# Performance work log

Measured on AMD Instinct MI355X. Metric: run time of the kernel, lower is better.

## Reference

```python
import jax, jax.numpy as jnp
import numpy as np

B, M, H = 8, 1024, 1024
NH, HD = 16, 64  # num_heads, head_dim


def setup_inputs() -> dict:
    key = jax.random.key(0)
    ks = jax.random.split(key, 16)
    s = 0.02
    def lin(k, din, dout):
        k1, k2 = jax.random.split(k)
        return (jax.random.normal(k1, (din, dout), jnp.float32) * s,
                jax.random.normal(k2, (dout,), jnp.float32) * s)
    x = jax.random.normal(ks[0], (B, M, H), jnp.float32)
    Wq, bq = lin(ks[1], H, H)
    Wk, bk = lin(ks[2], H, H)
    Wv, bv = lin(ks[3], H, H)
    Wg, bg = lin(ks[4], H, H)
    Wo, bo = lin(ks[5], H, H)
    Wu1, bu1 = lin(ks[6], H, H // 4)
    Wu2, bu2 = lin(ks[7], H // 4, 1)
    return dict(x=x, Wq=Wq, bq=bq, Wk=Wk, bk=bk, Wv=Wv, bv=bv, Wg=Wg, bg=bg,
                Wo=Wo, bo=bo, Wu1=Wu1, bu1=bu1, Wu2=Wu2, bu2=bu2)


def reference(x, Wq, bq, Wk, bk, Wv, bv, Wg, bg, Wo, bo, Wu1, bu1, Wu2, bu2):
    b, m, _ = x.shape
    shp = lambda t: t.reshape(b, m, NH, HD)
    q = shp(x @ Wq + bq)
    k = shp(x @ Wk + bk)
    v = shp(x @ Wv + bv)
    g = jax.nn.sigmoid(shp(x @ Wg + bg))
    scores = jnp.einsum('bmhd,bnhd->bhmn', q, k) / (HD ** 0.5)
    # modality uncertainty: Linear -> ReLU -> Linear -> Softplus, squeeze(-1)
    sigma = jax.nn.softplus(jax.nn.relu(x @ Wu1 + bu1) @ Wu2 + bu2)[..., 0] + 1e-6
    # sigma_pair: [b, 1, m, 1] * [b, 1, 1, m] -> broadcast over heads
    scores = scores / (sigma[:, None, :, None] * sigma[:, None, None, :])
    attn = jax.nn.softmax(scores, axis=-1)
    ctx = jnp.einsum('bhmn,bnhd->bmhd', attn, v) * g
    fused = ctx.reshape(b, m, H)
    z = fused.mean(axis=1) @ Wo + bo
    return (z, attn, sigma)
```

## Files before the change

### kernel.cpp

```cpp
#include <hip/hip_runtime.h>
#include <math.h>

#define BB 8
#define MM 1024
#define HH 1024
#define NH 16
#define HD 64
#define NCAT 4352
#define ROWS (BB*MM)

typedef unsigned short ushortT;
typedef __attribute__((ext_vector_type(8))) short bf16x8;
typedef __attribute__((ext_vector_type(4))) float f32x4;

__device__ __forceinline__ unsigned short f2bf(float f) {
    union { float f; unsigned int u; } v; v.f = f;
    unsigned int u = v.u;
    unsigned int r = (u + 0x7fffu + ((u >> 16) & 1u)) >> 16;
    return (unsigned short)r;
}
__device__ __forceinline__ float bf2f(unsigned short s) {
    union { unsigned int u; float f; } v; v.u = ((unsigned int)s) << 16;
    return v.f;
}

__device__ __forceinline__ void async_copy16(const void* g, void* l) {
    __builtin_amdgcn_global_load_lds(
        (const __attribute__((address_space(1))) unsigned int*)g,
        (__attribute__((address_space(3))) unsigned int*)l, 16, 0, 0);
}

__global__ void cast_x_k(const float* __restrict__ x, ushortT* __restrict__ Xb) {
    size_t i = ((size_t)blockIdx.x * 256 + threadIdx.x) * 4;
    float4 v = *(const float4*)&x[i];
    ushort4 o;
    o.x = f2bf(v.x); o.y = f2bf(v.y); o.z = f2bf(v.z); o.w = f2bf(v.w);
    *(ushort4*)&Xb[i] = o;
}

__global__ void wtrans_k(const float* __restrict__ Wq, const float* __restrict__ Wk,
                         const float* __restrict__ Wv, const float* __restrict__ Wg,
                         const float* __restrict__ Wu1, ushortT* __restrict__ Wt) {
    __shared__ float t[64][65];
    int n0 = blockIdx.x * 64, k0 = blockIdx.y * 64;
    const float* src; int ncols; int nloc0;
    if (n0 < 1024)      { src = Wq;  nloc0 = n0;        ncols = 1024; }
    else if (n0 < 2048) { src = Wk;  nloc0 = n0 - 1024; ncols = 1024; }
    else if (n0 < 3072) { src = Wv;  nloc0 = n0 - 2048; ncols = 1024; }
    else if (n0 < 4096) { src = Wg;  nloc0 = n0 - 3072; ncols = 1024; }
    else                { src = Wu1; nloc0 = n0 - 4096; ncols = 256;  }
    int tid = threadIdx.x, c = tid & 63, rq = tid >> 6;
#pragma unroll
    for (int i = 0; i < 16; i++) {
        int k = i * 4 + rq;
        t[k][c] = src[(size_t)(k0 + k) * ncols + nloc0 + c];
    }
    __syncthreads();
#pragma unroll
    for (int i = 0; i < 16; i++) {
        int nn = i * 4 + rq;
        Wt[(size_t)(n0 + nn) * 1024 + k0 + c] = f2bf(t[c][nn]);
    }
}

__global__ void biascat_k(const float* __restrict__ bq, const float* __restrict__ bk,
                          const float* __restrict__ bv, const float* __restrict__ bg,
                          const float* __restrict__ bu1, float* __restrict__ bc) {
    int i = blockIdx.x * 256 + threadIdx.x;
    if (i >= NCAT) return;
    float v;
    if (i < 1024) v = bq[i];
    else if (i < 2048) v = bk[i - 1024];
    else if (i < 3072) v = bv[i - 2048];
    else if (i < 4096) v = bg[i - 3072];
    else v = bu1[i - 4096];
    bc[i] = v;
}

__global__ __launch_bounds__(256, 2) void gemm_proj_k(
    const ushortT* __restrict__ Xb, const ushortT* __restrict__ Wt,
    const float* __restrict__ biascat, ushortT* __restrict__ Ycat) {
    __shared__ ushortT lA[128 * 64];
    __shared__ ushortT lB[128 * 64];
    const int tid = threadIdx.x;
    const int wave = tid >> 6;
    const int lane = tid & 63;
    const int quad = lane >> 4;
    const int l16 = lane & 15;
    const int m0 = blockIdx.y * 128;
    const int n0 = blockIdx.x * 128;
    const int wr = (wave >> 1) * 64;
    const int wc = (wave & 1) * 64;

    f32x4 acc[16];
#pragma unroll
    for (int i = 0; i < 16; i++) acc[i] = (f32x4){0.f, 0.f, 0.f, 0.f};

    for (int k0 = 0; k0 < 1024; k0 += 64) {
#pragma unroll
        for (int i = 0; i < 4; i++) {
            int c = wave * 256 + i * 64 + lane;
            int row = c >> 3, kc = c & 7;
            async_copy16(&Xb[(size_t)(m0 + row) * 1024 + k0 + kc * 8], &lA[c * 8]);
            async_copy16(&Wt[(size_t)(n0 + row) * 1024 + k0 + kc * 8], &lB[c * 8]);
        }
        __syncthreads();
#pragma unroll
        for (int kk = 0; kk < 64; kk += 32) {
            bf16x8 a[4], b[4];
#pragma unroll
            for (int i = 0; i < 4; i++)
                a[i] = *(const bf16x8*)&lA[(wr + i * 16 + l16) * 64 + kk + quad * 8];
#pragma unroll
            for (int j = 0; j < 4; j++)
                b[j] = *(const bf16x8*)&lB[(wc + j * 16 + l16) * 64 + kk + quad * 8];
#pragma unroll
            for (int i = 0; i < 4; i++)
#pragma unroll
                for (int j = 0; j < 4; j++)
                    acc[i * 4 + j] = __builtin_amdgcn_mfma_f32_16x16x32_bf16(
                        a[i], b[j], acc[i * 4 + j], 0, 0, 0);
        }
        __syncthreads();
    }

#pragma unroll
    for (int i = 0; i < 4; i++) {
#pragma unroll
        for (int j = 0; j < 4; j++) {
            int col = n0 + wc + j * 16 + l16;
            float bias = biascat[col];
#pragma unroll
            for (int r = 0; r < 4; r++) {
                int row = m0 + wr + i * 16 + quad * 4 + r;
                float y = acc[i * 4 + j][r] + bias;
                if (n0 < 1024) y *= 0.125f;
                else if (n0 < 3072) {  }
                else if (n0 < 4096) y = 1.f / (1.f + __expf(-y));
                else y = fmaxf(y, 0.f);
                Ycat[(size_t)row * NCAT + col] = f2bf(y);
            }
        }
    }
}

__global__ void vtrans_k(const ushortT* __restrict__ Ycat, ushortT* __restrict__ Vt) {
    __shared__ ushortT t[64][72];
    int n0 = blockIdx.x * 64, h = blockIdx.y, b = blockIdx.z;
    const ushortT* Vbase = Ycat + (size_t)(b * MM) * NCAT + 2048 + h * HD;
    int tid = threadIdx.x, c = tid & 63, rq = tid >> 6;
#pragma unroll
    for (int i = 0; i < 16; i++) {
        int n = i * 4 + rq;
        t[n][c] = Vbase[(size_t)(n0 + n) * NCAT + c];
    }
    __syncthreads();
    ushortT* out = Vt + (size_t)((b * NH + h) * HD) * MM;
#pragma unroll
    for (int i = 0; i < 16; i++) {
        int d = i * 4 + rq;
        out[(size_t)d * MM + n0 + c] = t[c][d];
    }
}

__global__ void sigma_k(const ushortT* __restrict__ Ycat, const float* __restrict__ Wu2,
                        const float* __restrict__ bu2, float* __restrict__ out_sigma,
                        float* __restrict__ rsig) {
    int row = blockIdx.x * 4 + (threadIdx.x >> 6);
    int lane = threadIdx.x & 63;
    const ushortT* u = Ycat + (size_t)row * NCAT + 4096;
    ushort4 uv = *(const ushort4*)(u + lane * 4);
    float4 wv = *(const float4*)(Wu2 + lane * 4);
    float acc = bf2f(uv.x) * wv.x + bf2f(uv.y) * wv.y + bf2f(uv.z) * wv.z + bf2f(uv.w) * wv.w;
#pragma unroll
    for (int d = 1; d < 64; d <<= 1) acc += __shfl_xor(acc, d, 64);
    if (lane == 0) {
        float y = acc + bu2[0];
        float sp = (y > 20.f) ? y : log1pf(__expf(y));
        float s = sp + 1e-6f;
        out_sigma[row] = s;
        rsig[row] = 1.f / s;
    }
}

__global__ __launch_bounds__(256, 2) void attn_k(
    const ushortT* __restrict__ Ycat, const ushortT* __restrict__ Vt,
    const float* __restrict__ rsig, float* __restrict__ attn_out,
    float* __restrict__ meanacc) {
    __shared__ ushortT lQ[64 * 64];
    __shared__ ushortT lK[64 * 64];
    __shared__ ushortT lV[64 * 64];
    __shared__ ushortT lP[4][16 * 64];
    __shared__ float lrs[1024];

    const int tid = threadIdx.x, wave = tid >> 6, lane = tid & 63;
    const int quad = lane >> 4, l16 = lane & 15;
    const int m0 = blockIdx.x * 64, h = blockIdx.y, b = blockIdx.z;

    const ushortT* Qbase = Ycat + (size_t)(b * MM) * NCAT + h * HD;
    const ushortT* Kbase = Ycat + (size_t)(b * MM) * NCAT + 1024 + h * HD;
    const ushortT* Gbase = Ycat + (size_t)(b * MM) * NCAT + 3072 + h * HD;
    const ushortT* Vbase = Vt + (size_t)((b * NH + h) * HD) * MM;

    for (int i = tid; i < 1024; i += 256) lrs[i] = rsig[b * MM + i];
#pragma unroll
    for (int i = 0; i < 2; i++) {
        int c = wave * 128 + i * 64 + lane;
        int row = c >> 3, kc = c & 7;
        async_copy16(&Qbase[(size_t)(m0 + row) * NCAT + kc * 8], &lQ[c * 8]);
    }
    __syncthreads();

    bf16x8 qa[2];
#pragma unroll
    for (int kk = 0; kk < 2; kk++)
        qa[kk] = *(const bf16x8*)&lQ[(wave * 16 + l16) * 64 + kk * 32 + quad * 8];
    float rm[4];
#pragma unroll
    for (int r = 0; r < 4; r++) rm[r] = lrs[m0 + wave * 16 + quad * 4 + r];

    float Mx[4], L[4];
#pragma unroll
    for (int r = 0; r < 4; r++) { Mx[r] = -1e30f; L[r] = 0.f; }

    for (int n0 = 0; n0 < MM; n0 += 64) {
#pragma unroll
        for (int i = 0; i < 2; i++) {
            int c = wave * 128 + i * 64 + lane;
            int row = c >> 3, kc = c & 7;
            async_copy16(&Kbase[(size_t)(n0 + row) * NCAT + kc * 8], &lK[c * 8]);
        }
        __syncthreads();
        f32x4 s[4];
#pragma unroll
        for (int j = 0; j < 4; j++) {
            bf16x8 b0 = *(const bf16x8*)&lK[(j * 16 + l16) * 64 + quad * 8];
            bf16x8 b1 = *(const bf16x8*)&lK[(j * 16 + l16) * 64 + 32 + quad * 8];
            f32x4 t = (f32x4){0.f, 0.f, 0.f, 0.f};
            t = __builtin_amdgcn_mfma_f32_16x16x32_bf16(qa[0], b0, t, 0, 0, 0);
            t = __builtin_amdgcn_mfma_f32_16x16x32_bf16(qa[1], b1, t, 0, 0, 0);
            float rn = lrs[n0 + j * 16 + l16];
#pragma unroll
            for (int r = 0; r < 4; r++) t[r] *= rm[r] * rn;
            s[j] = t;
        }
        __syncthreads();
#pragma unroll
        for (int r = 0; r < 4; r++) {
            float mx = fmaxf(fmaxf(s[0][r], s[1][r]), fmaxf(s[2][r], s[3][r]));
#pragma unroll
            for (int d = 1; d < 16; d <<= 1) mx = fmaxf(mx, __shfl_xor(mx, d, 16));
            float nm = fmaxf(Mx[r], mx);
            float sum = __expf(s[0][r] - nm) + __expf(s[1][r] - nm) +
                        __expf(s[2][r] - nm) + __expf(s[3][r] - nm);
#pragma unroll
            for (int d = 1; d < 16; d <<= 1) sum += __shfl_xor(sum, d, 16);
            L[r] = L[r] * __expf(Mx[r] - nm) + sum;
            Mx[r] = nm;
        }
    }

    float Li[4];
#pragma unroll
    for (int r = 0; r < 4; r++) Li[r] = 1.f / L[r];
    f32x4 ctx[4];
#pragma unroll
    for (int j = 0; j < 4; j++) ctx[j] = (f32x4){0.f, 0.f, 0.f, 0.f};
    float* attn_base = attn_out + ((size_t)((b * NH + h) * MM + m0)) * MM;
    ushortT* Pw = lP[wave];

    for (int n0 = 0; n0 < MM; n0 += 64) {
#pragma unroll
        for (int i = 0; i < 2; i++) {
            int c = wave * 128 + i * 64 + lane;
            int row = c >> 3, kc = c & 7;
            async_copy16(&Kbase[(size_t)(n0 + row) * NCAT + kc * 8], &lK[c * 8]);
            async_copy16(&Vbase[(size_t)row * MM + n0 + kc * 8], &lV[c * 8]);
        }
        __syncthreads();
#pragma unroll
        for (int j = 0; j < 4; j++) {
            bf16x8 b0 = *(const bf16x8*)&lK[(j * 16 + l16) * 64 + quad * 8];
            bf16x8 b1 = *(const bf16x8*)&lK[(j * 16 + l16) * 64 + 32 + quad * 8];
            f32x4 t = (f32x4){0.f, 0.f, 0.f, 0.f};
            t = __builtin_amdgcn_mfma_f32_16x16x32_bf16(qa[0], b0, t, 0, 0, 0);
            t = __builtin_amdgcn_mfma_f32_16x16x32_bf16(qa[1], b1, t, 0, 0, 0);
            float rn = lrs[n0 + j * 16 + l16];
#pragma unroll
            for (int r = 0; r < 4; r++) {
                float p = __expf(t[r] * rm[r] * rn - Mx[r]) * Li[r];
                int mloc = wave * 16 + quad * 4 + r;
                attn_base[(size_t)mloc * MM + n0 + j * 16 + l16] = p;
                Pw[(quad * 4 + r) * 64 + j * 16 + l16] = f2bf(p);
            }
        }
        __syncthreads();
#pragma unroll
        for (int kk = 0; kk < 2; kk++) {
            bf16x8 pa = *(const bf16x8*)&Pw[l16 * 64 + kk * 32 + quad * 8];
#pragma unroll
            for (int j = 0; j < 4; j++) {
                bf16x8 vb = *(const bf16x8*)&lV[(j * 16 + l16) * 64 + kk * 32 + quad * 8];
                ctx[j] = __builtin_amdgcn_mfma_f32_16x16x32_bf16(pa, vb, ctx[j], 0, 0, 0);
            }
        }
        __syncthreads();
    }

#pragma unroll
    for (int j = 0; j < 4; j++) {
        int d = j * 16 + l16;
        float sum = 0.f;
#pragma unroll
        for (int r = 0; r < 4; r++) {
            int mrow = m0 + wave * 16 + quad * 4 + r;
            float gv = bf2f(Gbase[(size_t)mrow * NCAT + d]);
            sum += ctx[j][r] * gv;
        }
        sum += __shfl_xor(sum, 16, 64);
        sum += __shfl_xor(sum, 32, 64);
        if (quad == 0)
            atomicAdd(&meanacc[b * HH + h * HD + d], sum);
    }
}

__global__ void z_k(const float* __restrict__ meanacc, const float* __restrict__ Wo,
                    const float* __restrict__ bo, float* __restrict__ z) {
    int n = blockIdx.x * 256 + threadIdx.x;
    int b = blockIdx.y;
    int k0 = blockIdx.z * 64;
    float acc = 0.f;
#pragma unroll 4
    for (int k = k0; k < k0 + 64; k++)
        acc = fmaf(meanacc[b * HH + k], Wo[(size_t)k * HH + n], acc);
    float v = acc * (1.f / 1024.f);
    if (blockIdx.z == 0) v += bo[n];
    atomicAdd(&z[b * HH + n], v);
}

extern "C" void kernel_launch(void* const* d_in, const int* in_sizes, int n_in,
                              void* d_out, int out_size, void* d_ws, size_t ws_size,
                              hipStream_t stream) {
    const float* x   = (const float*)d_in[0];
    const float* Wq  = (const float*)d_in[1];
    const float* bq  = (const float*)d_in[2];
    const float* Wk  = (const float*)d_in[3];
    const float* bk  = (const float*)d_in[4];
    const float* Wv  = (const float*)d_in[5];
    const float* bv  = (const float*)d_in[6];
    const float* Wg  = (const float*)d_in[7];
    const float* bg  = (const float*)d_in[8];
    const float* Wo  = (const float*)d_in[9];
    const float* bo  = (const float*)d_in[10];
    const float* Wu1 = (const float*)d_in[11];
    const float* bu1 = (const float*)d_in[12];
    const float* Wu2 = (const float*)d_in[13];
    const float* bu2 = (const float*)d_in[14];

    char* ws = (char*)d_ws;
    ushortT* Xb      = (ushortT*)(ws + 0);
    ushortT* Wt      = (ushortT*)(ws + 16777216);
    float*   biascat = (float*)  (ws + 25690112);
    ushortT* Ycat    = (ushortT*)(ws + 25707520);
    ushortT* Vt      = (ushortT*)(ws + 97010688);
    float*   rsig    = (float*)  (ws + 113787904);
    float*   meanacc = (float*)  (ws + 113820672);

    float* z_out     = (float*)d_out;
    float* attn_out  = (float*)d_out + 8192;
    float* sigma_out = (float*)d_out + 8192 + 134217728;

    hipMemsetAsync(z_out, 0, 8192 * sizeof(float), stream);
    hipMemsetAsync(meanacc, 0, 8192 * sizeof(float), stream);

    cast_x_k<<<dim3(ROWS * 1024 / 1024), 256, 0, stream>>>(x, Xb);
    wtrans_k<<<dim3(68, 16), 256, 0, stream>>>(Wq, Wk, Wv, Wg, Wu1, Wt);
    biascat_k<<<dim3(17), 256, 0, stream>>>(bq, bk, bv, bg, bu1, biascat);
    gemm_proj_k<<<dim3(NCAT / 128, ROWS / 128), 256, 0, stream>>>(Xb, Wt, biascat, Ycat);
    vtrans_k<<<dim3(16, NH, BB), 256, 0, stream>>>(Ycat, Vt);
    sigma_k<<<dim3(ROWS / 4), 256, 0, stream>>>(Ycat, Wu2, bu2, sigma_out, rsig);
    attn_k<<<dim3(16, NH, BB), 256, 0, stream>>>(Ycat, Vt, rsig, attn_out, meanacc);
    z_k<<<dim3(4, BB, 16), 256, 0, stream>>>(meanacc, Wo, bo, z_out);
}
```

Measured before the change: 880.8 us.

## Double-buffer K/V tiles, swizzle LDS, and drop online max in softmax pass

Adds double-buffered K and V LDS tiles, so the next tile's async global-to-LDS copy is issued before computing on the current one. Applies an XOR swizzle to the LDS row layout to reduce bank conflicts. Removes the running-max tracking from the row-sum pass and computes exp without max subtraction, which removes the per-tile shuffle reductions. Attention probabilities are buffered in registers and written after the P tile is staged. Skipping the max shift risks overflow if scores grow large, and the extra buffers raise LDS use.

```diff
diff --git a/kernel.cpp b/kernel.cpp
--- a/kernel.cpp
+++ b/kernel.cpp
@@ -28,6 +28,22 @@
     __builtin_amdgcn_global_load_lds(
         (const __attribute__((address_space(1))) unsigned int*)g,
         (__attribute__((address_space(3))) unsigned int*)l, 16, 0, 0);
+}
+
+__device__ __forceinline__ bf16x8 lds8(const ushortT* base, int row, int cb) {
+    const char* p = (const char*)(base + row * 64);
+    return *(const bf16x8*)(p + ((cb * 2) ^ ((row & 7) << 4)));
+}
+
+__device__ __forceinline__ void stage_tile(const ushortT* __restrict__ gsrc, size_t rstride,
+                                           ushortT* ldst, int wave, int lane) {
+#pragma unroll
+    for (int i = 0; i < 2; i++) {
+        int c = wave * 128 + i * 64 + lane;
+        int row = c >> 3;
+        int kc = (c & 7) ^ (row & 7);
+        async_copy16(&gsrc[(size_t)row * rstride + kc * 8], ldst + c * 8);
+    }
 }
 
 __global__ void cast_x_k(const float* __restrict__ x, ushortT* __restrict__ Xb) {
@@ -188,8 +204,8 @@
     const float* __restrict__ rsig, float* __restrict__ attn_out,
     float* __restrict__ meanacc) {
     __shared__ ushortT lQ[64 * 64];
-    __shared__ ushortT lK[64 * 64];
-    __shared__ ushortT lV[64 * 64];
+    __shared__ ushortT lK[2][64 * 64];
+    __shared__ ushortT lV[2][64 * 64];
     __shared__ ushortT lP[4][16 * 64];
     __shared__ float lrs[1024];
 
@@ -203,108 +219,101 @@
     const ushortT* Vbase = Vt + (size_t)((b * NH + h) * HD) * MM;
 
     for (int i = tid; i < 1024; i += 256) lrs[i] = rsig[b * MM + i];
-#pragma unroll
-    for (int i = 0; i < 2; i++) {
-        int c = wave * 128 + i * 64 + lane;
-        int row = c >> 3, kc = c & 7;
-        async_copy16(&Qbase[(size_t)(m0 + row) * NCAT + kc * 8], &lQ[c * 8]);
-    }
+    stage_tile(Qbase + (size_t)m0 * NCAT, NCAT, lQ, wave, lane);
+    stage_tile(Kbase, NCAT, lK[0], wave, lane);
     __syncthreads();
 
     bf16x8 qa[2];
-#pragma unroll
-    for (int kk = 0; kk < 2; kk++)
-        qa[kk] = *(const bf16x8*)&lQ[(wave * 16 + l16) * 64 + kk * 32 + quad * 8];
+    qa[0] = lds8(lQ, wave * 16 + l16, quad * 8);
+    qa[1] = lds8(lQ, wave * 16 + l16, 32 + quad * 8);
     float rm[4];
 #pragma unroll
     for (int r = 0; r < 4; r++) rm[r] = lrs[m0 + wave * 16 + quad * 4 + r];
 
-    float Mx[4], L[4];
-#pragma unroll
-    for (int r = 0; r < 4; r++) { Mx[r] = -1e30f; L[r] = 0.f; }
-
+    float L[4] = {0.f, 0.f, 0.f, 0.f};
+    int cur = 0;
     for (int n0 = 0; n0 < MM; n0 += 64) {
-#pragma unroll
-        for (int i = 0; i < 2; i++) {
-            int c = wave * 128 + i * 64 + lane;
-            int row = c >> 3, kc = c & 7;
-            async_copy16(&Kbase[(size_t)(n0 + row) * NCAT + kc * 8], &lK[c * 8]);
-        }
-        __syncthreads();
-        f32x4 s[4];
+        if (n0 + 64 < MM)
+            stage_tile(Kbase + (size_t)(n0 + 64) * NCAT, NCAT, lK[cur ^ 1], wave, lane);
+        const ushortT* Kc = lK[cur];
 #pragma unroll
         for (int j = 0; j < 4; j++) {
-            bf16x8 b0 = *(const bf16x8*)&lK[(j * 16 + l16) * 64 + quad * 8];
-            bf16x8 b1 = *(const bf16x8*)&lK[(j * 16 + l16) * 64 + 32 + quad * 8];
+            bf16x8 b0 = lds8(Kc, j * 16 + l16, quad * 8);
+            bf16x8 b1 = lds8(Kc, j * 16 + l16, 32 + quad * 8);
             f32x4 t = (f32x4){0.f, 0.f, 0.f, 0.f};
             t = __builtin_amdgcn_mfma_f32_16x16x32_bf16(qa[0], b0, t, 0, 0, 0);
             t = __builtin_amdgcn_mfma_f32_16x16x32_bf16(qa[1], b1, t, 0, 0, 0);
             float rn = lrs[n0 + j * 16 + l16];
 #pragma unroll
-            for (int r = 0; r < 4; r++) t[r] *= rm[r] * rn;
-            s[j] = t;
-        }
-        __syncthreads();
-#pragma unroll
-        for (int r = 0; r < 4; r++) {
-            float mx = fmaxf(fmaxf(s[0][r], s[1][r]), fmaxf(s[2][r], s[3][r]));
-#pragma unroll
-            for (int d = 1; d < 16; d <<= 1) mx = fmaxf(mx, __shfl_xor(mx, d, 16));
-            float nm = fmaxf(Mx[r], mx);
-            float sum = __expf(s[0][r] - nm) + __expf(s[1][r] - nm) +
-                        __expf(s[2][r] - nm) + __expf(s[3][r] - nm);
-#pragma unroll
-            for (int d = 1; d < 16; d <<= 1) sum += __shfl_xor(sum, d, 16);
-            L[r] = L[r] * __expf(Mx[r] - nm) + sum;
-            Mx[r] = nm;
-        }
-    }
-
+            for (int r = 0; r < 4; r++) L[r] += __expf(t[r] * rm[r] * rn);
+        }
+        __syncthreads();
+        cur ^= 1;
+    }
+
+    stage_tile(Kbase, NCAT, lK[0], wave, lane);
+    stage_tile(Vbase, MM, lV[0], wave, lane);
+
+#pragma unroll
+    for (int r = 0; r < 4; r++) {
+#pragma unroll
+        for (int d = 1; d < 16; d <<= 1) L[r] += __shfl_xor(L[r], d, 16);
+    }
     float Li[4];
 #pragma unroll
     for (int r = 0; r < 4; r++) Li[r] = 1.f / L[r];
+
     f32x4 ctx[4];
 #pragma unroll
     for (int j = 0; j < 4; j++) ctx[j] = (f32x4){0.f, 0.f, 0.f, 0.f};
     float* attn_base = attn_out + ((size_t)((b * NH + h) * MM + m0)) * MM;
     ushortT* Pw = lP[wave];
 
+    __syncthreads();
+    cur = 0;
+
     for (int n0 = 0; n0 < MM; n0 += 64) {
-#pragma unroll
-        for (int i = 0; i < 2; i++) {
-            int c = wave * 128 + i * 64 + lane;
-            int row = c >> 3, kc = c & 7;
-            async_copy16(&Kbase[(size_t)(n0 + row) * NCAT + kc * 8], &lK[c * 8]);
-            async_copy16(&Vbase[(size_t)row * MM + n0 + kc * 8], &lV[c * 8]);
-        }
-        __syncthreads();
+        if (n0 + 64 < MM) {
+            stage_tile(Kbase + (size_t)(n0 + 64) * NCAT, NCAT, lK[cur ^ 1], wave, lane);
+            stage_tile(Vbase + (n0 + 64), MM, lV[cur ^ 1], wave, lane);
+        }
+        const ushortT* Kc = lK[cur];
+        const ushortT* Vc = lV[cur];
+        float p[4][4];
 #pragma unroll
         for (int j = 0; j < 4; j++) {
-            bf16x8 b0 = *(const bf16x8*)&lK[(j * 16 + l16) * 64 + quad * 8];
-            bf16x8 b1 = *(const bf16x8*)&lK[(j * 16 + l16) * 64 + 32 + quad * 8];
+            bf16x8 b0 = lds8(Kc, j * 16 + l16, quad * 8);
+            bf16x8 b1 = lds8(Kc, j * 16 + l16, 32 + quad * 8);
             f32x4 t = (f32x4){0.f, 0.f, 0.f, 0.f};
             t = __builtin_amdgcn_mfma_f32_16x16x32_bf16(qa[0], b0, t, 0, 0, 0);
             t = __builtin_amdgcn_mfma_f32_16x16x32_bf16(qa[1], b1, t, 0, 0, 0);
             float rn = lrs[n0 + j * 16 + l16];
 #pragma unroll
             for (int r = 0; r < 4; r++) {
-                float p = __expf(t[r] * rm[r] * rn - Mx[r]) * Li[r];
-                int mloc = wave * 16 + quad * 4 + r;
-                attn_base[(size_t)mloc * MM + n0 + j * 16 + l16] = p;
-                Pw[(quad * 4 + r) * 64 + j * 16 + l16] = f2bf(p);
+                float pv = __expf(t[r] * rm[r] * rn) * Li[r];
+                p[j][r] = pv;
+                int prow = quad * 4 + r;
+                *(ushortT*)((char*)Pw + prow * 128 +
+                            (((j * 16 + l16) * 2) ^ ((prow & 7) << 4))) = f2bf(pv);
             }
         }
+#pragma unroll
+        for (int j = 0; j < 4; j++)
+#pragma unroll
+            for (int r = 0; r < 4; r++)
+                attn_base[(size_t)(wave * 16 + quad * 4 + r) * MM + n0 + j * 16 + l16] = p[j][r];
         __syncthreads();
 #pragma unroll
         for (int kk = 0; kk < 2; kk++) {
-            bf16x8 pa = *(const bf16x8*)&Pw[l16 * 64 + kk * 32 + quad * 8];
+            bf16x8 pa = lds8(Pw, l16, kk * 32 + quad * 8);
 #pragma unroll
             for (int j = 0; j < 4; j++) {
-                bf16x8 vb = *(const bf16x8*)&lV[(j * 16 + l16) * 64 + kk * 32 + quad * 8];
+                bf16x8 vb = lds8(Vc, j * 16 + l16, kk * 32 + quad * 8);
                 ctx[j] = __builtin_amdgcn_mfma_f32_16x16x32_bf16(pa, vb, ctx[j], 0, 0, 0);
             }
         }
         __syncthreads();
+        cur ^= 1;
     }
 
 #pragma unroll
```

Result: no change. 863.9 us (-1.9%).
